# Optimization experiments

Hardware: AMD Instinct MI355X
Metric: run time of the kernel (lower is better)

The kernel has to match this reference:

```python
import jax, jax.numpy as jnp
import numpy as np

N, E, IN_DIM, HID, HEADS, LAT = 50000, 800000, 128, 32, 4, 32


def _gat_params(key, fin, heads, cout):
    k1, k2, k3 = jax.random.split(key, 3)
    s = 1.0 / np.sqrt(fin)
    W = jax.random.uniform(k1, (fin, heads * cout), minval=-s, maxval=s, dtype=jnp.float32)
    a_src = jax.random.normal(k2, (heads, cout), dtype=jnp.float32) * 0.1
    a_dst = jax.random.normal(k3, (heads, cout), dtype=jnp.float32) * 0.1
    b = jnp.zeros((heads * cout,), dtype=jnp.float32)
    return W, a_src, a_dst, b


def setup_inputs() -> dict:
    key = jax.random.key(0)
    ks = jax.random.split(key, 8)
    x = jax.random.normal(ks[0], (N, IN_DIM), dtype=jnp.float32)
    edge_index = jax.random.randint(ks[1], (2, E), 0, N, dtype=jnp.int64)
    W1, a1s, a1d, b1 = _gat_params(ks[2], IN_DIM, HEADS, HID)
    W2, a2s, a2d, b2 = _gat_params(ks[3], HID * HEADS, HEADS, HID)
    Wl, als, ald, bl = _gat_params(ks[4], HID * HEADS, 1, LAT)
    Wd, ads_, add_, bd = _gat_params(ks[5], LAT, 1, HID)
    sdec = 1.0 / np.sqrt(HID)
    Wdec = jax.random.uniform(ks[6], (HID, IN_DIM), minval=-sdec, maxval=sdec, dtype=jnp.float32)
    bdec = jnp.zeros((IN_DIM,), dtype=jnp.float32)
    return {"x": x, "edge_index": edge_index,
            "W1": W1, "a1s": a1s, "a1d": a1d, "b1": b1,
            "W2": W2, "a2s": a2s, "a2d": a2d, "b2": b2,
            "Wl": Wl, "als": als, "ald": ald, "bl": bl,
            "Wd": Wd, "ads": ads_, "add": add_, "bd": bd,
            "Wdec": Wdec, "bdec": bdec}


def gat_conv(x, src, dst, W, a_s, a_d, b, n, concat=True):
    """PyG-style GATConv (eval mode, self-loops already in src/dst)."""
    H, C = a_s.shape
    h = (x @ W).reshape(n, H, C)                      # [N,H,C]
    alpha_src = jnp.sum(h * a_s, axis=-1)             # [N,H]
    alpha_dst = jnp.sum(h * a_d, axis=-1)             # [N,H]
    e = jax.nn.leaky_relu(alpha_src[src] + alpha_dst[dst], 0.2)  # [E,H]
    m = jax.ops.segment_max(e, dst, num_segments=n)
    m = jnp.where(jnp.isfinite(m), m, 0.0)
    ex = jnp.exp(e - m[dst])
    denom = jax.ops.segment_sum(ex, dst, num_segments=n)
    coef = ex / (denom[dst] + 1e-16)                  # [E,H]
    out = jax.ops.segment_sum(coef[:, :, None] * h[src], dst, num_segments=n)  # [N,H,C]
    out = out.reshape(n, H * C) if concat else out.mean(axis=1)
    return out + b


def reference(x, edge_index, W1, a1s, a1d, b1, W2, a2s, a2d, b2,
              Wl, als, ald, bl, Wd, ads, add, bd, Wdec, bdec):
    n = x.shape[0]
    # add self-loops (PyG GATConv default)
    loops = jnp.arange(n, dtype=edge_index.dtype)
    src = jnp.concatenate([edge_index[0], loops])
    dst = jnp.concatenate([edge_index[1], loops])
    lrelu = lambda v: jax.nn.leaky_relu(v, 0.01)
    x1 = lrelu(gat_conv(x, src, dst, W1, a1s, a1d, b1, n))
    x2 = lrelu(gat_conv(x1, src, dst, W2, a2s, a2d, b2, n))
    z = gat_conv(x2, src, dst, Wl, als, ald, bl, n)
    xr = lrelu(gat_conv(z, src, dst, Wd, ads, add, bd, n))
    reconstructed = xr @ Wdec + bdec + x
    return reconstructed, z
```

## Files before the change

kernel.cpp:

```cpp
#include <hip/hip_runtime.h>
#include <math.h>

#define CAP 64

typedef __attribute__((ext_vector_type(8))) short short8;
typedef __attribute__((ext_vector_type(4))) float f32x4;

__device__ __forceinline__ float lrelu02(float v) { return v > 0.f ? v : 0.2f * v; }
__device__ __forceinline__ float lrelu01(float v) { return v > 0.f ? v : 0.01f * v; }

__device__ __forceinline__ float bfl(unsigned u) { return __uint_as_float(u << 16); }
__device__ __forceinline__ float bfh(unsigned u) { return __uint_as_float(u & 0xffff0000u); }
__device__ __forceinline__ unsigned short f2bf(float f) {
  unsigned u = __float_as_uint(f);
  return (unsigned short)((u + 0x7fffu + ((u >> 16) & 1u)) >> 16);
}
__device__ __forceinline__ unsigned pk2bf(float lo, float hi) {
  return (unsigned)f2bf(lo) | ((unsigned)f2bf(hi) << 16);
}

template<int H>
__device__ __forceinline__ float selH(const float* a, int h) {
  float r = a[0];
#pragma unroll
  for (int i = 1; i < H; ++i) r = (h == i) ? a[i] : r;
  return r;
}

__global__ __launch_bounds__(256) void fill_k(const int* __restrict__ ei, int* __restrict__ deg,
                                              int* __restrict__ cols, int E) {
  int e = blockIdx.x * 256 + threadIdx.x;
  if (e >= E) return;
  int s = ei[e];
  int d = ei[E + e];
  int pos = atomicAdd(&deg[d], 1);
  if (pos < CAP) cols[(size_t)d * CAP + pos] = s;
}

__global__ __launch_bounds__(256) void cvtx_k(const float4* __restrict__ X, uint4* __restrict__ O, int n8) {
  int i = blockIdx.x * 256 + threadIdx.x;
  if (i >= n8) return;
  float4 a = X[2 * i], b = X[2 * i + 1];
  O[i] = make_uint4(pk2bf(a.x, a.y), pk2bf(a.z, a.w), pk2bf(b.x, b.y), pk2bf(b.z, b.w));
}

__global__ __launch_bounds__(256) void cvtw_k(const float* __restrict__ W1, const float* __restrict__ W2,
                                              const float* __restrict__ Wl, const float* __restrict__ Wd,
                                              const float* __restrict__ Wdec,
                                              unsigned short* __restrict__ t1, unsigned short* __restrict__ t2,
                                              unsigned short* __restrict__ tl, unsigned short* __restrict__ td,
                                              unsigned short* __restrict__ tdec) {
  int b = blockIdx.x, tid = threadIdx.x;
  const float* src; unsigned short* dst; int K, NC, base;
  if (b < 64)       { src = W1;   dst = t1;   K = 128; NC = 128; base = 0; }
  else if (b < 128) { src = W2;   dst = t2;   K = 128; NC = 128; base = 64; }
  else if (b < 144) { src = Wl;   dst = tl;   K = 128; NC = 32;  base = 128; }
  else if (b < 148) { src = Wd;   dst = td;   K = 32;  NC = 32;  base = 144; }
  else              { src = Wdec; dst = tdec; K = 32;  NC = 128; base = 148; }
  int e = (b - base) * 256 + tid;
  if (e < K * NC) {
    int k = e / NC, c = e - k * NC;
    dst[c * K + k] = f2bf(src[e]);
  }
}

template<int K, int NC, bool OUT16, bool ALPHA, bool RB>
__global__ __launch_bounds__(256) void gemm_mfma(const unsigned short* __restrict__ A,
                                                 const unsigned short* __restrict__ Wt,
                                                 const float* __restrict__ bias,
                                                 const float* __restrict__ resid,
                                                 void* __restrict__ Cv,
                                                 const float* __restrict__ a_s, const float* __restrict__ a_d,
                                                 float* __restrict__ asrc, float* __restrict__ adst, int M) {
  constexpr int BM = (NC == 128) ? 64 : 128;
  constexpr int NKS = K / 32;
  constexpr int RS = (NC == 128) ? 4 : 2;
  constexpr int SWZ = (K == 128) ? 7 : 3;
  constexpr int CH = BM * K / 2048;
  __shared__ unsigned short At[BM * K];
  const int tid = threadIdx.x;
  const int wid = tid >> 6, lane = tid & 63;
  const int g = lane >> 4, l15 = lane & 15;
  const int row0 = blockIdx.x * BM;

  short8 wf[NKS][2];
  const int cglob0 = ((NC == 128) ? 32 * wid : 0) + l15;
#pragma unroll
  for (int ks = 0; ks < NKS; ++ks)
#pragma unroll
    for (int cf = 0; cf < 2; ++cf)
      wf[ks][cf] = *(const short8*)(Wt + (size_t)(cglob0 + 16 * cf) * K + ks * 32 + g * 8);

  uint4 ra[CH];
#pragma unroll
  for (int c = 0; c < CH; ++c) {
    int ch = c * 256 + tid;
    int row = ch * 8 / K;
    ra[c] = (row0 + row < M) ? *(const uint4*)(A + (size_t)row0 * K + ch * 8)
                             : make_uint4(0u, 0u, 0u, 0u);
  }
#pragma unroll
  for (int c = 0; c < CH; ++c) {
    int ch = c * 256 + tid;
    int row = ch * 8 / K;
    int off = ch * 16 - row * (2 * K);
    *(uint4*)((char*)At + row * (2 * K) + (off ^ ((row & SWZ) << 4))) = ra[c];
  }
  __syncthreads();

  f32x4 acc[RS][2];
#pragma unroll
  for (int r = 0; r < RS; ++r)
#pragma unroll
    for (int cf = 0; cf < 2; ++cf) acc[r][cf] = (f32x4){0.f, 0.f, 0.f, 0.f};

  const int rwave = (NC == 128) ? 0 : 32 * wid;
#pragma unroll
  for (int ks = 0; ks < NKS; ++ks) {
#pragma unroll
    for (int r = 0; r < RS; ++r) {
      int row = rwave + 16 * r + l15;
      int off = ks * 64 + g * 16;
      short8 af = *(const short8*)((const char*)At + row * (2 * K) + (off ^ ((row & SWZ) << 4)));
#pragma unroll
      for (int cf = 0; cf < 2; ++cf)
        acc[r][cf] = __builtin_amdgcn_mfma_f32_16x16x32_bf16(wf[ks][cf], af, acc[r][cf], 0, 0, 0);
    }
  }

#pragma unroll
  for (int r = 0; r < RS; ++r) {
    const int row = row0 + rwave + 16 * r + l15;
    const bool ok = row < M;
#pragma unroll
    for (int cf = 0; cf < 2; ++cf) {
      const int colbase = ((NC == 128) ? 32 * wid : 0) + 16 * cf + 4 * g;
      if constexpr (OUT16) {
        if (ok) {
          unsigned short* Cb = (unsigned short*)Cv;
          ushort4 o;
          o.x = f2bf(acc[r][cf][0]); o.y = f2bf(acc[r][cf][1]);
          o.z = f2bf(acc[r][cf][2]); o.w = f2bf(acc[r][cf][3]);
          *(ushort4*)(Cb + (size_t)row * NC + colbase) = o;
        }
      } else if constexpr (RB) {
        if (ok) {
          float* C = (float*)Cv;
          float4 bi = *(const float4*)(bias + colbase);
          float4 rv = *(const float4*)(resid + (size_t)row * NC + colbase);
          float4 o;
          o.x = acc[r][cf][0] + bi.x + rv.x;
          o.y = acc[r][cf][1] + bi.y + rv.y;
          o.z = acc[r][cf][2] + bi.z + rv.z;
          o.w = acc[r][cf][3] + bi.w + rv.w;
          *(float4*)(C + (size_t)row * NC + colbase) = o;
        }
      }
    }
    if constexpr (ALPHA) {
      constexpr int H = NC / 32;
      const int head = (NC == 128) ? wid : 0;
      float ps = 0.f, pd = 0.f;
#pragma unroll
      for (int cf = 0; cf < 2; ++cf) {
        float4 sa = *(const float4*)(a_s + head * 32 + 16 * cf + 4 * g);
        float4 da = *(const float4*)(a_d + head * 32 + 16 * cf + 4 * g);
        ps += acc[r][cf][0] * sa.x + acc[r][cf][1] * sa.y + acc[r][cf][2] * sa.z + acc[r][cf][3] * sa.w;
        pd += acc[r][cf][0] * da.x + acc[r][cf][1] * da.y + acc[r][cf][2] * da.z + acc[r][cf][3] * da.w;
      }
      ps += __shfl_xor(ps, 16, 64); pd += __shfl_xor(pd, 16, 64);
      ps += __shfl_xor(ps, 32, 64); pd += __shfl_xor(pd, 32, 64);
      if (g == 0 && ok) {
        asrc[(size_t)row * H + head] = ps;
        adst[(size_t)row * H + head] = pd;
      }
    }
  }
}

template<int ACT>
__global__ __launch_bounds__(256) void agg128_k(const unsigned short* __restrict__ Hb,
                                                const float4* __restrict__ asrc4,
                                                const float4* __restrict__ adst4,
                                                const int* __restrict__ deg, const int* __restrict__ cols,
                                                const float* __restrict__ bias,
                                                unsigned short* __restrict__ Y, int Nn) {
  __shared__ float wl[4][256];
  __shared__ int sl[4][64];
  const int wid = threadIdx.x >> 6, lane = threadIdx.x & 63;
  const int node = blockIdx.x * 4 + wid;
  if (node >= Nn) return;
  float4 ad = adst4[node], as_ = asrc4[node];
  const float adr[4] = {ad.x, ad.y, ad.z, ad.w};
  const float asr[4] = {as_.x, as_.y, as_.z, as_.w};
  int cnt = deg[node];
  cnt = cnt > CAP ? CAP : cnt;
  const int* __restrict__ cl = cols + (size_t)node * CAP;
  int s = (lane < cnt) ? cl[lane] : 0;
  float4 av = asrc4[s];
  const float asv[4] = {av.x, av.y, av.z, av.w};
  float w[4], dn[4];
#pragma unroll
  for (int h = 0; h < 4; ++h) {
    w[h] = (lane < cnt) ? __expf(lrelu02(asv[h] + adr[h])) : 0.f;
    dn[h] = w[h];
  }
#pragma unroll
  for (int off = 32; off >= 1; off >>= 1)
#pragma unroll
    for (int h = 0; h < 4; ++h) dn[h] += __shfl_xor(dn[h], off, 64);
  float wnself[4], inv[4];
#pragma unroll
  for (int h = 0; h < 4; ++h) {
    float ws = __expf(lrelu02(asr[h] + adr[h]));
    dn[h] += ws;
    inv[h] = 1.f / (dn[h] + 1e-16f);
    wnself[h] = ws * inv[h];
  }
  float4 wn = {w[0] * inv[0], w[1] * inv[1], w[2] * inv[2], w[3] * inv[3]};
  *(float4*)&wl[wid][lane * 4] = wn;
  sl[wid][lane] = s * 16;
  __builtin_amdgcn_wave_barrier();

  const uint4* __restrict__ HB = (const uint4*)Hb;
  const int sub = lane >> 4;
  const int c8 = lane & 15;
  const int h = c8 >> 2;
  float a0 = 0.f, a1 = 0.f, a2 = 0.f, a3 = 0.f, a4 = 0.f, a5 = 0.f, a6 = 0.f, a7 = 0.f;
  float p0 = 0.f, p1 = 0.f, p2 = 0.f, p3 = 0.f, p4 = 0.f, p5 = 0.f, p6 = 0.f, p7 = 0.f;
  int i = sub;
  for (; i + 4 < cnt; i += 8) {
    int o0 = sl[wid][i];
    int o1 = sl[wid][i + 4];
    float w0 = wl[wid][i * 4 + h];
    float w1 = wl[wid][(i + 4) * 4 + h];
    uint4 u0 = HB[o0 + c8];
    uint4 u1 = HB[o1 + c8];
    a0 += w0 * bfl(u0.x); a1 += w0 * bfh(u0.x); a2 += w0 * bfl(u0.y); a3 += w0 * bfh(u0.y);
    a4 += w0 * bfl(u0.z); a5 += w0 * bfh(u0.z); a6 += w0 * bfl(u0.w); a7 += w0 * bfh(u0.w);
    p0 += w1 * bfl(u1.x); p1 += w1 * bfh(u1.x); p2 += w1 * bfl(u1.y); p3 += w1 * bfh(u1.y);
    p4 += w1 * bfl(u1.z); p5 += w1 * bfh(u1.z); p6 += w1 * bfl(u1.w); p7 += w1 * bfh(u1.w);
  }
  for (; i < cnt; i += 4) {
    int o0 = sl[wid][i];
    float w0 = wl[wid][i * 4 + h];
    uint4 u0 = HB[o0 + c8];
    a0 += w0 * bfl(u0.x); a1 += w0 * bfh(u0.x); a2 += w0 * bfl(u0.y); a3 += w0 * bfh(u0.y);
    a4 += w0 * bfl(u0.z); a5 += w0 * bfh(u0.z); a6 += w0 * bfl(u0.w); a7 += w0 * bfh(u0.w);
  }
  a0 += p0; a1 += p1; a2 += p2; a3 += p3; a4 += p4; a5 += p5; a6 += p6; a7 += p7;
#pragma unroll
  for (int off = 16; off <= 32; off <<= 1) {
    a0 += __shfl_xor(a0, off, 64); a1 += __shfl_xor(a1, off, 64);
    a2 += __shfl_xor(a2, off, 64); a3 += __shfl_xor(a3, off, 64);
    a4 += __shfl_xor(a4, off, 64); a5 += __shfl_xor(a5, off, 64);
    a6 += __shfl_xor(a6, off, 64); a7 += __shfl_xor(a7, off, 64);
  }
  if (lane < 16) {
    uint4 us = HB[node * 16 + c8];
    float wns = selH<4>(wnself, h);
    float4 b0 = *(const float4*)(bias + c8 * 8);
    float4 b1 = *(const float4*)(bias + c8 * 8 + 4);
    float o0 = a0 + wns * bfl(us.x) + b0.x;
    float o1 = a1 + wns * bfh(us.x) + b0.y;
    float o2 = a2 + wns * bfl(us.y) + b0.z;
    float o3 = a3 + wns * bfh(us.y) + b0.w;
    float o4 = a4 + wns * bfl(us.z) + b1.x;
    float o5 = a5 + wns * bfh(us.z) + b1.y;
    float o6 = a6 + wns * bfl(us.w) + b1.z;
    float o7 = a7 + wns * bfh(us.w) + b1.w;
    if (ACT == 1) {
      o0 = lrelu01(o0); o1 = lrelu01(o1); o2 = lrelu01(o2); o3 = lrelu01(o3);
      o4 = lrelu01(o4); o5 = lrelu01(o5); o6 = lrelu01(o6); o7 = lrelu01(o7);
    }
    ((uint4*)Y)[(size_t)node * 16 + c8] =
        make_uint4(pk2bf(o0, o1), pk2bf(o2, o3), pk2bf(o4, o5), pk2bf(o6, o7));
  }
}

template<int ACT, int OMODE>
__global__ __launch_bounds__(256) void agg32_k(const unsigned short* __restrict__ Hb,
                                               const float* __restrict__ asrc, const float* __restrict__ adst,
                                               const int* __restrict__ deg, const int* __restrict__ cols,
                                               const float* __restrict__ bias, void* __restrict__ Yv,
                                               void* __restrict__ Yv2, int Nn) {
  __shared__ float wl[4][64];
  __shared__ int sl[4][64];
  const int wid = threadIdx.x >> 6, lane = threadIdx.x & 63;
  const int node = blockIdx.x * 4 + wid;
  if (node >= Nn) return;
  const float adr = adst[node], asr = asrc[node];
  int cnt = deg[node];
  cnt = cnt > CAP ? CAP : cnt;
  const int* __restrict__ cl = cols + (size_t)node * CAP;
  int s = (lane < cnt) ? cl[lane] : 0;
  float w = (lane < cnt) ? __expf(lrelu02(asrc[s] + adr)) : 0.f;
  float dn = w;
#pragma unroll
  for (int off = 32; off >= 1; off >>= 1) dn += __shfl_xor(dn, off, 64);
  float ws = __expf(lrelu02(asr + adr));
  dn += ws;
  float inv = 1.f / (dn + 1e-16f);
  wl[wid][lane] = w * inv;
  sl[wid][lane] = s * 8;
  __builtin_amdgcn_wave_barrier();

  const uint2* __restrict__ HB = (const uint2*)Hb;
  const int sub = lane >> 3;
  const int c = lane & 7;
  float a0 = 0.f, a1 = 0.f, a2 = 0.f, a3 = 0.f;
  float p0 = 0.f, p1 = 0.f, p2 = 0.f, p3 = 0.f;
  int i = sub;
  for (; i + 8 < cnt; i += 16) {
    int o0 = sl[wid][i];
    int o1 = sl[wid][i + 8];
    float w0 = wl[wid][i];
    float w1 = wl[wid][i + 8];
    uint2 u0 = HB[o0 + c];
    uint2 u1 = HB[o1 + c];
    a0 += w0 * bfl(u0.x); a1 += w0 * bfh(u0.x); a2 += w0 * bfl(u0.y); a3 += w0 * bfh(u0.y);
    p0 += w1 * bfl(u1.x); p1 += w1 * bfh(u1.x); p2 += w1 * bfl(u1.y); p3 += w1 * bfh(u1.y);
  }
  for (; i < cnt; i += 8) {
    int o0 = sl[wid][i];
    float w0 = wl[wid][i];
    uint2 u0 = HB[o0 + c];
    a0 += w0 * bfl(u0.x); a1 += w0 * bfh(u0.x); a2 += w0 * bfl(u0.y); a3 += w0 * bfh(u0.y);
  }
  a0 += p0; a1 += p1; a2 += p2; a3 += p3;
#pragma unroll
  for (int off = 8; off <= 32; off <<= 1) {
    a0 += __shfl_xor(a0, off, 64); a1 += __shfl_xor(a1, off, 64);
    a2 += __shfl_xor(a2, off, 64); a3 += __shfl_xor(a3, off, 64);
  }
  if (lane < 8) {
    uint2 us = HB[node * 8 + c];
    float wns = ws * inv;
    float4 bb = ((const float4*)bias)[c];
    float o0 = a0 + wns * bfl(us.x) + bb.x;
    float o1 = a1 + wns * bfh(us.x) + bb.y;
    float o2 = a2 + wns * bfl(us.y) + bb.z;
    float o3 = a3 + wns * bfh(us.y) + bb.w;
    if (ACT == 1) { o0 = lrelu01(o0); o1 = lrelu01(o1); o2 = lrelu01(o2); o3 = lrelu01(o3); }
    if constexpr (OMODE == 2) {
      ((float4*)Yv)[(size_t)node * 8 + c] = make_float4(o0, o1, o2, o3);
      ((uint2*)Yv2)[(size_t)node * 8 + c] = make_uint2(pk2bf(o0, o1), pk2bf(o2, o3));
    } else {
      ((uint2*)Yv)[(size_t)node * 8 + c] = make_uint2(pk2bf(o0, o1), pk2bf(o2, o3));
    }
  }
}

extern "C" void kernel_launch(void* const* d_in, const int* in_sizes, int n_in,
                              void* d_out, int out_size, void* d_ws, size_t ws_size,
                              hipStream_t stream) {
  const float* x = (const float*)d_in[0];
  const int* ei = (const int*)d_in[1];
  const float* W1 = (const float*)d_in[2];
  const float* a1s = (const float*)d_in[3];
  const float* a1d = (const float*)d_in[4];
  const float* b1 = (const float*)d_in[5];
  const float* W2 = (const float*)d_in[6];
  const float* a2s = (const float*)d_in[7];
  const float* a2d = (const float*)d_in[8];
  const float* b2 = (const float*)d_in[9];
  const float* Wl = (const float*)d_in[10];
  const float* als = (const float*)d_in[11];
  const float* ald = (const float*)d_in[12];
  const float* bl = (const float*)d_in[13];
  const float* Wd = (const float*)d_in[14];
  const float* ads = (const float*)d_in[15];
  const float* add_ = (const float*)d_in[16];
  const float* bd = (const float*)d_in[17];
  const float* Wdec = (const float*)d_in[18];
  const float* bdec = (const float*)d_in[19];

  const int N = in_sizes[0] / 128;
  const int E = in_sizes[1] / 2;

  char* ws = (char*)d_ws;
  auto alloc = [&](size_t bytes) {
    char* p = ws;
    ws += (bytes + 255) & ~(size_t)255;
    return p;
  };
  int* cols = (int*)alloc((size_t)N * CAP * 4);
  int* deg = (int*)alloc((size_t)N * 4);
  unsigned short* hb16 = (unsigned short*)alloc((size_t)N * 128 * 2);
  float* asrc = (float*)alloc((size_t)N * 4 * 4);
  float* adst = (float*)alloc((size_t)N * 4 * 4);
  unsigned short* x12 = (unsigned short*)alloc((size_t)N * 128 * 2);
  unsigned short* x16 = (unsigned short*)alloc((size_t)N * 128 * 2);
  unsigned short* z16 = (unsigned short*)alloc((size_t)N * 32 * 2);
  unsigned short* xr16 = (unsigned short*)alloc((size_t)N * 32 * 2);
  unsigned short* W1t = (unsigned short*)alloc(128 * 128 * 2);
  unsigned short* W2t = (unsigned short*)alloc(128 * 128 * 2);
  unsigned short* Wlt = (unsigned short*)alloc(128 * 32 * 2);
  unsigned short* Wdt = (unsigned short*)alloc(32 * 32 * 2);
  unsigned short* Wdect = (unsigned short*)alloc(32 * 128 * 2);

  float* rec = (float*)d_out;
  float* zout = (float*)d_out + (size_t)N * 128;

  hipMemsetAsync(deg, 0, (size_t)N * 4, stream);
  fill_k<<<(E + 255) / 256, 256, 0, stream>>>(ei, deg, cols, E);
  cvtx_k<<<(N * 128 / 8 + 255) / 256, 256, 0, stream>>>((const float4*)x, (uint4*)x16, N * 128 / 8);
  cvtw_k<<<164, 256, 0, stream>>>(W1, W2, Wl, Wd, Wdec, W1t, W2t, Wlt, Wdt, Wdect);

  const int gG128 = (N + 63) / 64;
  const int gG32 = (N + 127) / 128;
  const int gAg = (N + 3) / 4;

  gemm_mfma<128, 128, true, true, false><<<gG128, 256, 0, stream>>>(
      x16, W1t, nullptr, nullptr, hb16, a1s, a1d, asrc, adst, N);
  agg128_k<1><<<gAg, 256, 0, stream>>>(hb16, (const float4*)asrc, (const float4*)adst, deg, cols, b1, x12, N);

  gemm_mfma<128, 128, true, true, false><<<gG128, 256, 0, stream>>>(
      x12, W2t, nullptr, nullptr, hb16, a2s, a2d, asrc, adst, N);
  agg128_k<1><<<gAg, 256, 0, stream>>>(hb16, (const float4*)asrc, (const float4*)adst, deg, cols, b2, x12, N);

  gemm_mfma<128, 32, true, true, false><<<gG32, 256, 0, stream>>>(
      x12, Wlt, nullptr, nullptr, hb16, als, ald, asrc, adst, N);
  agg32_k<0, 2><<<gAg, 256, 0, stream>>>(hb16, asrc, adst, deg, cols, bl, zout, z16, N);

  gemm_mfma<32, 32, true, true, false><<<gG32, 256, 0, stream>>>(
      z16, Wdt, nullptr, nullptr, hb16, ads, add_, asrc, adst, N);
  agg32_k<1, 1><<<gAg, 256, 0, stream>>>(hb16, asrc, adst, deg, cols, bd, xr16, nullptr, N);

  gemm_mfma<32, 128, false, false, true><<<gG128, 256, 0, stream>>>(
      xr16, Wdect, bdec, x, rec, nullptr, nullptr, nullptr, nullptr, N);
}
```

Before: 389.9 us.

## Fuse x bf16 conversion into first GEMM, use 16-bit column indices, restructure agg128 weights

Drops the separate cvtx kernel: the first GEMM now loads fp32 x directly and packs it to bf16 on the fly. Neighbor column indices are stored as unsigned short instead of int, which halves the adjacency traffic. This relies on N (50000) fitting in 16 bits, so it only holds for node counts up to 65535. agg128 now computes per-edge, per-head attention weights with one lane per (edge, head) pair looping over 16-edge chunks instead of float4 per lane, and normalizes the weights in shared memory.

```diff
diff --git a/kernel.cpp b/kernel.cpp
--- a/kernel.cpp
+++ b/kernel.cpp
@@ -19,29 +19,14 @@
   return (unsigned)f2bf(lo) | ((unsigned)f2bf(hi) << 16);
 }
 
-template<int H>
-__device__ __forceinline__ float selH(const float* a, int h) {
-  float r = a[0];
-#pragma unroll
-  for (int i = 1; i < H; ++i) r = (h == i) ? a[i] : r;
-  return r;
-}
-
 __global__ __launch_bounds__(256) void fill_k(const int* __restrict__ ei, int* __restrict__ deg,
-                                              int* __restrict__ cols, int E) {
+                                              unsigned short* __restrict__ cols, int E) {
   int e = blockIdx.x * 256 + threadIdx.x;
   if (e >= E) return;
   int s = ei[e];
   int d = ei[E + e];
   int pos = atomicAdd(&deg[d], 1);
-  if (pos < CAP) cols[(size_t)d * CAP + pos] = s;
-}
-
-__global__ __launch_bounds__(256) void cvtx_k(const float4* __restrict__ X, uint4* __restrict__ O, int n8) {
-  int i = blockIdx.x * 256 + threadIdx.x;
-  if (i >= n8) return;
-  float4 a = X[2 * i], b = X[2 * i + 1];
-  O[i] = make_uint4(pk2bf(a.x, a.y), pk2bf(a.z, a.w), pk2bf(b.x, b.y), pk2bf(b.z, b.w));
+  if (pos < CAP) cols[(size_t)d * CAP + pos] = (unsigned short)s;
 }
 
 __global__ __launch_bounds__(256) void cvtw_k(const float* __restrict__ W1, const float* __restrict__ W2,
@@ -64,8 +49,8 @@
   }
 }
 
-template<int K, int NC, bool OUT16, bool ALPHA, bool RB>
-__global__ __launch_bounds__(256) void gemm_mfma(const unsigned short* __restrict__ A,
+template<int K, int NC, bool OUT16, bool ALPHA, bool RB, bool IN32>
+__global__ __launch_bounds__(256) void gemm_mfma(const void* __restrict__ Av,
                                                  const unsigned short* __restrict__ Wt,
                                                  const float* __restrict__ bias,
                                                  const float* __restrict__ resid,
@@ -92,12 +77,29 @@
       wf[ks][cf] = *(const short8*)(Wt + (size_t)(cglob0 + 16 * cf) * K + ks * 32 + g * 8);
 
   uint4 ra[CH];
-#pragma unroll
-  for (int c = 0; c < CH; ++c) {
-    int ch = c * 256 + tid;
-    int row = ch * 8 / K;
-    ra[c] = (row0 + row < M) ? *(const uint4*)(A + (size_t)row0 * K + ch * 8)
-                             : make_uint4(0u, 0u, 0u, 0u);
+  if constexpr (IN32) {
+    const float* Af = (const float*)Av;
+#pragma unroll
+    for (int c = 0; c < CH; ++c) {
+      int ch = c * 256 + tid;
+      int row = ch * 8 / K;
+      int col = ch * 8 - row * K;
+      float4 lo = {0.f, 0.f, 0.f, 0.f}, hi = {0.f, 0.f, 0.f, 0.f};
+      if (row0 + row < M) {
+        lo = *(const float4*)(Af + (size_t)(row0 + row) * K + col);
+        hi = *(const float4*)(Af + (size_t)(row0 + row) * K + col + 4);
+      }
+      ra[c] = make_uint4(pk2bf(lo.x, lo.y), pk2bf(lo.z, lo.w), pk2bf(hi.x, hi.y), pk2bf(hi.z, hi.w));
+    }
+  } else {
+    const unsigned short* Ab = (const unsigned short*)Av;
+#pragma unroll
+    for (int c = 0; c < CH; ++c) {
+      int ch = c * 256 + tid;
+      int row = ch * 8 / K;
+      ra[c] = (row0 + row < M) ? *(const uint4*)(Ab + (size_t)row0 * K + ch * 8)
+                               : make_uint4(0u, 0u, 0u, 0u);
+    }
   }
 #pragma unroll
   for (int c = 0; c < CH; ++c) {
@@ -180,9 +182,10 @@
 
 template<int ACT>
 __global__ __launch_bounds__(256) void agg128_k(const unsigned short* __restrict__ Hb,
-                                                const float4* __restrict__ asrc4,
-                                                const float4* __restrict__ adst4,
-                                                const int* __restrict__ deg, const int* __restrict__ cols,
+                                                const float* __restrict__ asrc,
+                                                const float* __restrict__ adst,
+                                                const int* __restrict__ deg,
+                                                const unsigned short* __restrict__ cols,
                                                 const float* __restrict__ bias,
                                                 unsigned short* __restrict__ Y, int Nn) {
   __shared__ float wl[4][256];
@@ -190,36 +193,32 @@
   const int wid = threadIdx.x >> 6, lane = threadIdx.x & 63;
   const int node = blockIdx.x * 4 + wid;
   if (node >= Nn) return;
-  float4 ad = adst4[node], as_ = asrc4[node];
-  const float adr[4] = {ad.x, ad.y, ad.z, ad.w};
-  const float asr[4] = {as_.x, as_.y, as_.z, as_.w};
+  const int eidx = lane >> 2, h4 = lane & 3;
+  const float adr = adst[node * 4 + h4];
+  const float asr = asrc[node * 4 + h4];
   int cnt = deg[node];
   cnt = cnt > CAP ? CAP : cnt;
-  const int* __restrict__ cl = cols + (size_t)node * CAP;
-  int s = (lane < cnt) ? cl[lane] : 0;
-  float4 av = asrc4[s];
-  const float asv[4] = {av.x, av.y, av.z, av.w};
-  float w[4], dn[4];
-#pragma unroll
-  for (int h = 0; h < 4; ++h) {
-    w[h] = (lane < cnt) ? __expf(lrelu02(asv[h] + adr[h])) : 0.f;
-    dn[h] = w[h];
-  }
-#pragma unroll
-  for (int off = 32; off >= 1; off >>= 1)
-#pragma unroll
-    for (int h = 0; h < 4; ++h) dn[h] += __shfl_xor(dn[h], off, 64);
-  float wnself[4], inv[4];
-#pragma unroll
-  for (int h = 0; h < 4; ++h) {
-    float ws = __expf(lrelu02(asr[h] + adr[h]));
-    dn[h] += ws;
-    inv[h] = 1.f / (dn[h] + 1e-16f);
-    wnself[h] = ws * inv[h];
-  }
-  float4 wn = {w[0] * inv[0], w[1] * inv[1], w[2] * inv[2], w[3] * inv[3]};
-  *(float4*)&wl[wid][lane * 4] = wn;
-  sl[wid][lane] = s * 16;
+  const unsigned short* __restrict__ cl = cols + (size_t)node * CAP;
+  float dn = 0.f;
+  for (int c0 = 0; c0 < cnt; c0 += 16) {
+    int e = c0 + eidx;
+    bool valid = e < cnt;
+    int s = valid ? (int)cl[e] : 0;
+    float w = valid ? __expf(lrelu02(asrc[s * 4 + h4] + adr)) : 0.f;
+    wl[wid][e * 4 + h4] = w;
+    if (h4 == 0) sl[wid][e] = s * 16;
+    dn += w;
+  }
+  dn += __shfl_xor(dn, 4, 64);
+  dn += __shfl_xor(dn, 8, 64);
+  dn += __shfl_xor(dn, 16, 64);
+  dn += __shfl_xor(dn, 32, 64);
+  float wself = __expf(lrelu02(asr + adr));
+  dn += wself;
+  float inv = 1.f / (dn + 1e-16f);
+  float wsinv = wself * inv;
+  for (int j = lane; j < cnt * 4; j += 64) wl[wid][j] *= inv;
+  float wns = __shfl(wsinv, (lane & 15) >> 2, 64);
   __builtin_amdgcn_wave_barrier();
 
   const uint4* __restrict__ HB = (const uint4*)Hb;
@@ -258,7 +257,6 @@
   }
   if (lane < 16) {
     uint4 us = HB[node * 16 + c8];
-    float wns = selH<4>(wnself, h);
     float4 b0 = *(const float4*)(bias + c8 * 8);
     float4 b1 = *(const float4*)(bias + c8 * 8 + 4);
     float o0 = a0 + wns * bfl(us.x) + b0.x;
@@ -281,7 +279,8 @@
 template<int ACT, int OMODE>
 __global__ __launch_bounds__(256) void agg32_k(const unsigned short* __restrict__ Hb,
                                                const float* __restrict__ asrc, const float* __restrict__ adst,
-                                               const int* __restrict__ deg, const int* __restrict__ cols,
+                                               const int* __restrict__ deg,
+                                               const unsigned short* __restrict__ cols,
                                                const float* __restrict__ bias, void* __restrict__ Yv,
                                                void* __restrict__ Yv2, int Nn) {
   __shared__ float wl[4][64];
@@ -292,8 +291,8 @@
   const float adr = adst[node], asr = asrc[node];
   int cnt = deg[node];
   cnt = cnt > CAP ? CAP : cnt;
-  const int* __restrict__ cl = cols + (size_t)node * CAP;
-  int s = (lane < cnt) ? cl[lane] : 0;
+  const unsigned short* __restrict__ cl = cols + (size_t)node * CAP;
+  int s = (lane < cnt) ? (int)cl[lane] : 0;
   float w = (lane < cnt) ? __expf(lrelu02(asrc[s] + adr)) : 0.f;
   float dn = w;
 #pragma unroll
@@ -384,13 +383,12 @@
     ws += (bytes + 255) & ~(size_t)255;
     return p;
   };
-  int* cols = (int*)alloc((size_t)N * CAP * 4);
+  unsigned short* cols = (unsigned short*)alloc((size_t)N * CAP * 2);
   int* deg = (int*)alloc((size_t)N * 4);
   unsigned short* hb16 = (unsigned short*)alloc((size_t)N * 128 * 2);
   float* asrc = (float*)alloc((size_t)N * 4 * 4);
   float* adst = (float*)alloc((size_t)N * 4 * 4);
   unsigned short* x12 = (unsigned short*)alloc((size_t)N * 128 * 2);
-  unsigned short* x16 = (unsigned short*)alloc((size_t)N * 128 * 2);
   unsigned short* z16 = (unsigned short*)alloc((size_t)N * 32 * 2);
   unsigned short* xr16 = (unsigned short*)alloc((size_t)N * 32 * 2);
   unsigned short* W1t = (unsigned short*)alloc(128 * 128 * 2);
@@ -404,29 +402,28 @@
 
   hipMemsetAsync(deg, 0, (size_t)N * 4, stream);
   fill_k<<<(E + 255) / 256, 256, 0, stream>>>(ei, deg, cols, E);
-  cvtx_k<<<(N * 128 / 8 + 255) / 256, 256, 0, stream>>>((const float4*)x, (uint4*)x16, N * 128 / 8);
   cvtw_k<<<164, 256, 0, stream>>>(W1, W2, Wl, Wd, Wdec, W1t, W2t, Wlt, Wdt, Wdect);
 
   const int gG128 = (N + 63) / 64;
   const int gG32 = (N + 127) / 128;
   const int gAg = (N + 3) / 4;
 
-  gemm_mfma<128, 128, true, true, false><<<gG128, 256, 0, stream>>>(
-      x16, W1t, nullptr, nullptr, hb16, a1s, a1d, asrc, adst, N);
-  agg128_k<1><<<gAg, 256, 0, stream>>>(hb16, (const float4*)asrc, (const float4*)adst, deg, cols, b1, x12, N);
-
-  gemm_mfma<128, 128, true, true, false><<<gG128, 256, 0, stream>>>(
+  gemm_mfma<128, 128, true, true, false, true><<<gG128, 256, 0, stream>>>(
+      x, W1t, nullptr, nullptr, hb16, a1s, a1d, asrc, adst, N);
+  agg128_k<1><<<gAg, 256, 0, stream>>>(hb16, asrc, adst, deg, cols, b1, x12, N);
+
+  gemm_mfma<128, 128, true, true, false, false><<<gG128, 256, 0, stream>>>(
       x12, W2t, nullptr, nullptr, hb16, a2s, a2d, asrc, adst, N);
-  agg128_k<1><<<gAg, 256, 0, stream>>>(hb16, (const float4*)asrc, (const float4*)adst, deg, cols, b2, x12, N);
-
-  gemm_mfma<128, 32, true, true, false><<<gG32, 256, 0, stream>>>(
+  agg128_k<1><<<gAg, 256, 0, stream>>>(hb16, asrc, adst, deg, cols, b2, x12, N);
+
+  gemm_mfma<128, 32, true, true, false, false><<<gG32, 256, 0, stream>>>(
       x12, Wlt, nullptr, nullptr, hb16, als, ald, asrc, adst, N);
   agg32_k<0, 2><<<gAg, 256, 0, stream>>>(hb16, asrc, adst, deg, cols, bl, zout, z16, N);
 
-  gemm_mfma<32, 32, true, true, false><<<gG32, 256, 0, stream>>>(
+  gemm_mfma<32, 32, true, true, false, false><<<gG32, 256, 0, stream>>>(
       z16, Wdt, nullptr, nullptr, hb16, ads, add_, asrc, adst, N);
   agg32_k<1, 1><<<gAg, 256, 0, stream>>>(hb16, asrc, adst, deg, cols, bd, xr16, nullptr, N);
 
-  gemm_mfma<32, 128, false, false, true><<<gG128, 256, 0, stream>>>(
+  gemm_mfma<32, 128, false, false, true, false><<<gG128, 256, 0, stream>>>(
       xr16, Wdect, bdec, x, rec, nullptr, nullptr, nullptr, nullptr, N);
 }
```

Result: faster. 332.6 us (-14.7%).
